# Kernel optimization log

Hardware: AMD Instinct MI355X
Metric: run time of the kernel (lower is better)

## Reference

```python
import jax, jax.numpy as jnp
import numpy as np

B, I, J, C = 1, 320, 320, 128
H, Dh = 4, 32
AH = H * Dh  # all_head_size == 128
EPS = 1e-5


def setup_inputs() -> dict:
    key = jax.random.key(0)
    ks = jax.random.split(key, 10)
    s = 0.05
    return {
        "z": jax.random.normal(ks[0], (B, I, J, C), jnp.float32),
        "z_mask": jax.random.randint(ks[1], (B, I, J), 0, 2, jnp.int32),
        "ln_scale": jnp.ones((C,), jnp.float32),
        "ln_bias": jnp.zeros((C,), jnp.float32),
        "Wq": jax.random.normal(ks[2], (C, AH), jnp.float32) * s,
        "Wk": jax.random.normal(ks[3], (C, AH), jnp.float32) * s,
        "Wv": jax.random.normal(ks[4], (C, AH), jnp.float32) * s,
        "Wg": jax.random.normal(ks[5], (C, AH), jnp.float32) * s,
        "bg": jnp.zeros((AH,), jnp.float32),
        "Wo": jax.random.normal(ks[6], (AH, C), jnp.float32) * s,
        "bo": jnp.zeros((C,), jnp.float32),
    }


def _layernorm(x, scale, bias):
    mu = jnp.mean(x, axis=-1, keepdims=True)
    var = jnp.var(x, axis=-1, keepdims=True)
    return (x - mu) * jax.lax.rsqrt(var + EPS) * scale + bias


def reference(z, z_mask, ln_scale, ln_bias, Wq, Wk, Wv, Wg, bg, Wo, bo):
    zn = _layernorm(z, ln_scale, ln_bias)                  # [B,I,J,C]
    m = z_mask.astype(jnp.float32)                         # [B,I,J]
    mask_bias = 1e9 * (m - 1.0)[:, :, None, None, :]       # [B,I,1,1,J]

    def heads(x):
        return x.reshape(x.shape[:-1] + (H, Dh))

    q = heads(zn @ Wq)                                     # [B,I,J,H,Dh]
    k = heads(zn @ Wk)
    v = heads(zn @ Wv)
    # NOTE: original module applies NO 1/sqrt(d) scaling — faithful.
    logits = jnp.einsum('biqhc,bikhc->bihqk', q, k) + mask_bias
    weights = jax.nn.softmax(logits, axis=-1)              # [B,I,H,J,J]
    wa = jnp.einsum('bihqk,bikhc->biqhc', weights, v)      # [B,I,J,H,Dh]
    g = jax.nn.sigmoid(heads(zn @ Wg + bg))                # [B,I,J,H,Dh]
    out = (g * wa).reshape(z.shape[:-1] + (AH,))           # [B,I,J,AH]
    return (out @ Wo + bo) * m[..., None]                  # [B,I,J,C]
```

## Files before the change

kernel.cpp:

```cpp
#include <hip/hip_runtime.h>

typedef _Float16 f16;
typedef _Float16 f16x2 __attribute__((ext_vector_type(2)));
typedef _Float16 f16x4 __attribute__((ext_vector_type(4)));
typedef _Float16 f16x8 __attribute__((ext_vector_type(8)));
typedef float f32x4 __attribute__((ext_vector_type(4)));

#define I_DIM 320
#define J_DIM 320
#define C_DIM 128
#define NROWS (I_DIM * J_DIM)
#define LOG2E 1.44269504f

__device__ inline float pkrtz(float a, float b) {
    return __builtin_bit_cast(float, __builtin_amdgcn_cvt_pkrtz(a, b));
}

__global__ __launch_bounds__(256) void prep_kernel(const float* __restrict__ Wq,
                                                   const float* __restrict__ Wk,
                                                   const float* __restrict__ Wv,
                                                   const float* __restrict__ Wg,
                                                   const float* __restrict__ Wo,
                                                   f16* __restrict__ Wfrag) {
    int f = blockIdx.x * 256 + threadIdx.x;
    int j = f & 7, lane = (f >> 3) & 63, n = (f >> 9) & 7;
    int ks = (f >> 12) & 3, w = f >> 14;
    int gq = lane >> 4, r16 = lane & 15;
    const float* W = (w == 0) ? Wq : (w == 1) ? Wk : (w == 2) ? Wv : (w == 3) ? Wg : Wo;
    float val = W[(size_t)(ks * 32 + gq * 8 + j) * 128 + n * 16 + r16];
    if (w == 0) val *= LOG2E;
    Wfrag[f] = (f16)val;
}

__global__ __launch_bounds__(256) void ln_kernel(const float* __restrict__ z,
                                                 const float* __restrict__ scale,
                                                 const float* __restrict__ bias,
                                                 f16* __restrict__ zn) {
    int s = blockIdx.x;
    int b = (s & 7) * 3200 + (s >> 3);
    int wave = threadIdx.x >> 6;
    int lane = threadIdx.x & 63;
    int row = b * 4 + wave;
    const float* zr = z + (size_t)row * C_DIM;
    float2 x = *(const float2*)(zr + lane * 2);
    float sm = x.x + x.y;
    float sq = x.x * x.x + x.y * x.y;
    #pragma unroll
    for (int o = 32; o; o >>= 1) {
        sm += __shfl_xor(sm, o);
        sq += __shfl_xor(sq, o);
    }
    float mu = sm * (1.0f / 128.0f);
    float var = sq * (1.0f / 128.0f) - mu * mu;
    float rs = rsqrtf(var + 1e-5f);
    int c0 = lane * 2;
    float y0 = (x.x - mu) * rs * scale[c0] + bias[c0];
    float y1 = (x.y - mu) * rs * scale[c0 + 1] + bias[c0 + 1];
    f16x2 o2 = {(f16)y0, (f16)y1};
    *(f16x2*)(zn + (size_t)row * C_DIM + c0) = o2;
}

__global__ __launch_bounds__(256, 3) void attn_mega(const f16* __restrict__ zn,
                                                    const f16* __restrict__ Wfrag,
                                                    const float* __restrict__ bg,
                                                    const int* __restrict__ z_mask,
                                                    f16* __restrict__ gwa) {
    __shared__ f16 Ksh[320][40];
    __shared__ f16 Vt[32][328];
    __shared__ float mbs[320];

    int bid = blockIdx.x;
    int xcd = bid & 7, idx = bid >> 3;
    int i = xcd * 40 + (idx >> 2);
    int h = idx & 3;
    size_t zbase = (size_t)i * (J_DIM * C_DIM);
    size_t gbase = zbase + h * 32;

    int wave = threadIdx.x >> 6;
    int lane = threadIdx.x & 63;
    int gq = lane >> 4, r16 = lane & 15;

    const f16* wfq = Wfrag;
    const f16* wfk = Wfrag + 16384;
    const f16* wfv = Wfrag + 32768;
    const f16* wfg = Wfrag + 49152;

    for (int t = threadIdx.x; t < 320; t += 256)
        mbs[t] = z_mask[i * J_DIM + t] ? -12.0f : -60000.0f;

    for (int rt = wave; rt < 20; rt += 4) {
        f16x8 a[4];
        #pragma unroll
        for (int ks = 0; ks < 4; ++ks)
            a[ks] = *(const f16x8*)(zn + zbase + (size_t)(rt * 16 + r16) * C_DIM + ks * 32 + gq * 8);
        f32x4 kacc[2] = {}, vacc[2] = {};
        #pragma unroll
        for (int ks = 0; ks < 4; ++ks) {
            #pragma unroll
            for (int n = 0; n < 2; ++n) {
                f16x8 bk = *(const f16x8*)(wfk + (ks * 8 + 2 * h + n) * 512 + lane * 8);
                kacc[n] = __builtin_amdgcn_mfma_f32_16x16x32_f16(a[ks], bk, kacc[n], 0, 0, 0);
                f16x8 bv = *(const f16x8*)(wfv + (ks * 8 + 2 * h + n) * 512 + lane * 8);
                vacc[n] = __builtin_amdgcn_mfma_f32_16x16x32_f16(a[ks], bv, vacc[n], 0, 0, 0);
            }
        }
        int kcol = (r16 >> 2) * 8 + (r16 & 3);
        int colbase = (rt >> 1) * 32 + gq * 8 + (rt & 1) * 4;
        #pragma unroll
        for (int n = 0; n < 2; ++n) {
            #pragma unroll
            for (int rr = 0; rr < 4; ++rr)
                Ksh[rt * 16 + gq * 4 + rr][kcol + 4 * n] = (f16)kacc[n][rr];
            f16x4 vp = {(f16)vacc[n][0], (f16)vacc[n][1], (f16)vacc[n][2], (f16)vacc[n][3]};
            *(f16x4*)(&Vt[n * 16 + r16][colbase]) = vp;
        }
    }
    __syncthreads();

    f16x8 qa[5];
    f32x4 gacc[5][2] = {};
    #pragma unroll
    for (int u = 0; u < 5; ++u) {
        int qt = u * 4 + wave;
        f16x8 a[4];
        #pragma unroll
        for (int ks = 0; ks < 4; ++ks)
            a[ks] = *(const f16x8*)(zn + zbase + (size_t)(qt * 16 + r16) * C_DIM + ks * 32 + gq * 8);
        f32x4 qacc[2] = {};
        #pragma unroll
        for (int ks = 0; ks < 4; ++ks) {
            #pragma unroll
            for (int n = 0; n < 2; ++n) {
                f16x8 bq = *(const f16x8*)(wfq + (ks * 8 + 2 * h + n) * 512 + lane * 8);
                qacc[n] = __builtin_amdgcn_mfma_f32_16x16x32_f16(bq, a[ks], qacc[n], 0, 0, 0);
                f16x8 bgf = *(const f16x8*)(wfg + (ks * 8 + 2 * h + n) * 512 + lane * 8);
                gacc[u][n] = __builtin_amdgcn_mfma_f32_16x16x32_f16(a[ks], bgf, gacc[u][n], 0, 0, 0);
            }
        }
        union { float f[4]; f16x8 v; } qu;
        qu.f[0] = pkrtz(qacc[0][0], qacc[0][1]);
        qu.f[1] = pkrtz(qacc[0][2], qacc[0][3]);
        qu.f[2] = pkrtz(qacc[1][0], qacc[1][1]);
        qu.f[3] = pkrtz(qacc[1][2], qacc[1][3]);
        qa[u] = qu.v;
    }

    const f16x8 ones = {(f16)1, (f16)1, (f16)1, (f16)1, (f16)1, (f16)1, (f16)1, (f16)1};
    f32x4 wa[5][2] = {};
    f32x4 wa2[5] = {};

    #pragma unroll 2
    for (int kc = 0; kc < 10; ++kc) {
        f16x8 kb0 = *(const f16x8*)(&Ksh[kc * 32 + r16][gq * 8]);
        f16x8 kb1 = *(const f16x8*)(&Ksh[kc * 32 + 16 + r16][gq * 8]);
        f32x4 mk0 = *(const f32x4*)(&mbs[kc * 32 + 4 * gq]);
        f32x4 mk1 = *(const f32x4*)(&mbs[kc * 32 + 16 + 4 * gq]);
        f16x8 vb0 = *(const f16x8*)(&Vt[r16][kc * 32 + gq * 8]);
        f16x8 vb1 = *(const f16x8*)(&Vt[16 + r16][kc * 32 + gq * 8]);
        #pragma unroll
        for (int u = 0; u < 5; ++u) {
            f32x4 sc0 = __builtin_amdgcn_mfma_f32_16x16x32_f16(kb0, qa[u], mk0, 0, 0, 0);
            f32x4 sc1 = __builtin_amdgcn_mfma_f32_16x16x32_f16(kb1, qa[u], mk1, 0, 0, 0);
            float p0[4], p1[4];
            #pragma unroll
            for (int r = 0; r < 4; ++r) {
                p0[r] = __builtin_amdgcn_exp2f(sc0[r]);
                p1[r] = __builtin_amdgcn_exp2f(sc1[r]);
            }
            union { float f[4]; f16x8 v; } pu;
            pu.f[0] = pkrtz(p0[0], p0[1]);
            pu.f[1] = pkrtz(p0[2], p0[3]);
            pu.f[2] = pkrtz(p1[0], p1[1]);
            pu.f[3] = pkrtz(p1[2], p1[3]);
            wa[u][0] = __builtin_amdgcn_mfma_f32_16x16x32_f16(pu.v, vb0, wa[u][0], 0, 0, 0);
            wa[u][1] = __builtin_amdgcn_mfma_f32_16x16x32_f16(pu.v, vb1, wa[u][1], 0, 0, 0);
            wa2[u]   = __builtin_amdgcn_mfma_f32_16x16x32_f16(pu.v, ones, wa2[u], 0, 0, 0);
        }
    }

    float bgv0 = bg[h * 32 + r16];
    float bgv1 = bg[h * 32 + 16 + r16];
    #pragma unroll
    for (int u = 0; u < 5; ++u) {
        int qt = u * 4 + wave;
        float rinv[4];
        #pragma unroll
        for (int r = 0; r < 4; ++r)
            rinv[r] = 1.0f / wa2[u][r];
        #pragma unroll
        for (int n = 0; n < 2; ++n) {
            float bgn = n ? bgv1 : bgv0;
            #pragma unroll
            for (int r = 0; r < 4; ++r) {
                int jq = qt * 16 + gq * 4 + r;
                int dh = n * 16 + r16;
                float gv = 1.0f / (1.0f + __expf(-(gacc[u][n][r] + bgn)));
                gwa[gbase + (size_t)jq * C_DIM + dh] = (f16)(gv * wa[u][n][r] * rinv[r]);
            }
        }
    }
}

__global__ __launch_bounds__(256) void out_kernel(const f16* __restrict__ gwa,
                                                  const f16* __restrict__ Wofrag,
                                                  const float* __restrict__ bo,
                                                  const int* __restrict__ z_mask,
                                                  float* __restrict__ out) {
    int s = blockIdx.x;
    int b = (s & 7) * 50 + (s >> 3);
    int wave = threadIdx.x >> 6;
    int lane = threadIdx.x & 63;
    int gq = lane >> 4, r16 = lane & 15;
    int row0 = b * 256 + wave * 64;

    f32x4 acc[4][8] = {};
    #pragma unroll
    for (int ks = 0; ks < 4; ++ks) {
        f16x8 a[4];
        #pragma unroll
        for (int m = 0; m < 4; ++m)
            a[m] = *(const f16x8*)(gwa + (size_t)(row0 + m * 16 + r16) * C_DIM + ks * 32 + gq * 8);
        #pragma unroll
        for (int n = 0; n < 8; ++n) {
            f16x8 bb = *(const f16x8*)(Wofrag + (ks * 8 + n) * 512 + lane * 8);
            #pragma unroll
            for (int m = 0; m < 4; ++m)
                acc[m][n] = __builtin_amdgcn_mfma_f32_16x16x32_f16(a[m], bb, acc[m][n], 0, 0, 0);
        }
    }
    #pragma unroll
    for (int m = 0; m < 4; ++m) {
        #pragma unroll
        for (int rr = 0; rr < 4; ++rr) {
            int row = row0 + m * 16 + gq * 4 + rr;
            float mk = (float)z_mask[row];
            #pragma unroll
            for (int n = 0; n < 8; ++n) {
                int col = n * 16 + r16;
                out[(size_t)row * C_DIM + col] = (acc[m][n][rr] + bo[col]) * mk;
            }
        }
    }
}

extern "C" void kernel_launch(void* const* d_in, const int* in_sizes, int n_in,
                              void* d_out, int out_size, void* d_ws, size_t ws_size,
                              hipStream_t stream) {
    const float* z        = (const float*)d_in[0];
    const int*   z_mask   = (const int*)d_in[1];
    const float* ln_scale = (const float*)d_in[2];
    const float* ln_bias  = (const float*)d_in[3];
    const float* Wq       = (const float*)d_in[4];
    const float* Wk       = (const float*)d_in[5];
    const float* Wv       = (const float*)d_in[6];
    const float* Wg       = (const float*)d_in[7];
    const float* bg       = (const float*)d_in[8];
    const float* Wo       = (const float*)d_in[9];
    const float* bo       = (const float*)d_in[10];
    float* out = (float*)d_out;

    char* ws = (char*)d_ws;
    const size_t SZ = (size_t)NROWS * C_DIM * sizeof(f16);
    f16* zn    = (f16*)(ws);
    f16* gwa   = (f16*)(ws + 1 * SZ);
    f16* Wfrag = (f16*)(ws + 2 * SZ);

    prep_kernel<<<320, 256, 0, stream>>>(Wq, Wk, Wv, Wg, Wo, Wfrag);
    ln_kernel  <<<NROWS / 4, 256, 0, stream>>>(z, ln_scale, ln_bias, zn);
    attn_mega  <<<I_DIM * 4, 256, 0, stream>>>(zn, Wfrag, bg, z_mask, gwa);
    out_kernel <<<NROWS / 256, 256, 0, stream>>>(gwa, Wfrag + 4 * 16384, bo, z_mask, out);
}
```

Measured before the change: 98.36 us.

## Fuse LayerNorm into attention kernel, computing MFMA fragments from fp32 z

Removes the standalone LayerNorm kernel and the fp16 zn workspace. The attention kernel now loads fp32 z rows directly and normalizes them in registers while building the MFMA A fragments, with scale and bias staged in shared memory. This drops one launch and a full write and reread of the normalized tensor. In exchange, each block reads twice as many bytes per row, redundantly recomputes LN statistics across the four head blocks and both passes, and raises register pressure.

```diff
diff --git a/kernel.cpp b/kernel.cpp
--- a/kernel.cpp
+++ b/kernel.cpp
@@ -14,6 +14,42 @@
 
 __device__ inline float pkrtz(float a, float b) {
     return __builtin_bit_cast(float, __builtin_amdgcn_cvt_pkrtz(a, b));
+}
+
+__device__ __forceinline__ void ln_frags(const float* __restrict__ zr,
+                                         const float* __restrict__ scf,
+                                         const float* __restrict__ bif,
+                                         int gq, f16x8 a[4]) {
+    float4 zv[8];
+    #pragma unroll
+    for (int ks = 0; ks < 4; ++ks) {
+        zv[2 * ks]     = *(const float4*)(zr + ks * 32 + gq * 8);
+        zv[2 * ks + 1] = *(const float4*)(zr + ks * 32 + gq * 8 + 4);
+    }
+    float s = 0.0f, sq = 0.0f;
+    #pragma unroll
+    for (int t = 0; t < 8; ++t) {
+        float4 v = zv[t];
+        s  += v.x + v.y + v.z + v.w;
+        sq += v.x * v.x + v.y * v.y + v.z * v.z + v.w * v.w;
+    }
+    s  += __shfl_xor(s, 16);  s  += __shfl_xor(s, 32);
+    sq += __shfl_xor(sq, 16); sq += __shfl_xor(sq, 32);
+    float mu = s * (1.0f / 128.0f);
+    float var = sq * (1.0f / 128.0f) - mu * mu;
+    float rs = rsqrtf(var + 1e-5f);
+    #pragma unroll
+    for (int ks = 0; ks < 4; ++ks) {
+        int c0 = ks * 32 + gq * 8;
+        f16x8 av;
+        #pragma unroll
+        for (int j = 0; j < 8; ++j) {
+            float zj = (j < 4) ? ((const float*)&zv[2 * ks])[j]
+                               : ((const float*)&zv[2 * ks + 1])[j - 4];
+            av[j] = (f16)((zj - mu) * rs * scf[c0 + j] + bif[c0 + j]);
+        }
+        a[ks] = av;
+    }
 }
 
 __global__ __launch_bounds__(256) void prep_kernel(const float* __restrict__ Wq,
@@ -32,35 +68,9 @@
     Wfrag[f] = (f16)val;
 }
 
-__global__ __launch_bounds__(256) void ln_kernel(const float* __restrict__ z,
-                                                 const float* __restrict__ scale,
-                                                 const float* __restrict__ bias,
-                                                 f16* __restrict__ zn) {
-    int s = blockIdx.x;
-    int b = (s & 7) * 3200 + (s >> 3);
-    int wave = threadIdx.x >> 6;
-    int lane = threadIdx.x & 63;
-    int row = b * 4 + wave;
-    const float* zr = z + (size_t)row * C_DIM;
-    float2 x = *(const float2*)(zr + lane * 2);
-    float sm = x.x + x.y;
-    float sq = x.x * x.x + x.y * x.y;
-    #pragma unroll
-    for (int o = 32; o; o >>= 1) {
-        sm += __shfl_xor(sm, o);
-        sq += __shfl_xor(sq, o);
-    }
-    float mu = sm * (1.0f / 128.0f);
-    float var = sq * (1.0f / 128.0f) - mu * mu;
-    float rs = rsqrtf(var + 1e-5f);
-    int c0 = lane * 2;
-    float y0 = (x.x - mu) * rs * scale[c0] + bias[c0];
-    float y1 = (x.y - mu) * rs * scale[c0 + 1] + bias[c0 + 1];
-    f16x2 o2 = {(f16)y0, (f16)y1};
-    *(f16x2*)(zn + (size_t)row * C_DIM + c0) = o2;
-}
-
-__global__ __launch_bounds__(256, 3) void attn_mega(const f16* __restrict__ zn,
+__global__ __launch_bounds__(256, 3) void attn_mega(const float* __restrict__ z,
+                                                    const float* __restrict__ ln_scale,
+                                                    const float* __restrict__ ln_bias,
                                                     const f16* __restrict__ Wfrag,
                                                     const float* __restrict__ bg,
                                                     const int* __restrict__ z_mask,
@@ -68,13 +78,14 @@
     __shared__ f16 Ksh[320][40];
     __shared__ f16 Vt[32][328];
     __shared__ float mbs[320];
+    __shared__ float scf[128];
+    __shared__ float bif[128];
 
     int bid = blockIdx.x;
     int xcd = bid & 7, idx = bid >> 3;
     int i = xcd * 40 + (idx >> 2);
     int h = idx & 3;
-    size_t zbase = (size_t)i * (J_DIM * C_DIM);
-    size_t gbase = zbase + h * 32;
+    size_t gbase = (size_t)i * (J_DIM * C_DIM) + h * 32;
 
     int wave = threadIdx.x >> 6;
     int lane = threadIdx.x & 63;
@@ -87,12 +98,16 @@
 
     for (int t = threadIdx.x; t < 320; t += 256)
         mbs[t] = z_mask[i * J_DIM + t] ? -12.0f : -60000.0f;
+    for (int t = threadIdx.x; t < 128; t += 256) {
+        scf[t] = ln_scale[t];
+        bif[t] = ln_bias[t];
+    }
+    __syncthreads();
 
     for (int rt = wave; rt < 20; rt += 4) {
+        const float* zr = z + ((size_t)i * J_DIM + rt * 16 + r16) * C_DIM;
         f16x8 a[4];
-        #pragma unroll
-        for (int ks = 0; ks < 4; ++ks)
-            a[ks] = *(const f16x8*)(zn + zbase + (size_t)(rt * 16 + r16) * C_DIM + ks * 32 + gq * 8);
+        ln_frags(zr, scf, bif, gq, a);
         f32x4 kacc[2] = {}, vacc[2] = {};
         #pragma unroll
         for (int ks = 0; ks < 4; ++ks) {
@@ -122,10 +137,9 @@
     #pragma unroll
     for (int u = 0; u < 5; ++u) {
         int qt = u * 4 + wave;
+        const float* zr = z + ((size_t)i * J_DIM + qt * 16 + r16) * C_DIM;
         f16x8 a[4];
-        #pragma unroll
-        for (int ks = 0; ks < 4; ++ks)
-            a[ks] = *(const f16x8*)(zn + zbase + (size_t)(qt * 16 + r16) * C_DIM + ks * 32 + gq * 8);
+        ln_frags(zr, scf, bif, gq, a);
         f32x4 qacc[2] = {};
         #pragma unroll
         for (int ks = 0; ks < 4; ++ks) {
@@ -261,12 +275,10 @@
 
     char* ws = (char*)d_ws;
     const size_t SZ = (size_t)NROWS * C_DIM * sizeof(f16);
-    f16* zn    = (f16*)(ws);
-    f16* gwa   = (f16*)(ws + 1 * SZ);
-    f16* Wfrag = (f16*)(ws + 2 * SZ);
+    f16* gwa   = (f16*)(ws);
+    f16* Wfrag = (f16*)(ws + SZ);
 
     prep_kernel<<<320, 256, 0, stream>>>(Wq, Wk, Wv, Wg, Wo, Wfrag);
-    ln_kernel  <<<NROWS / 4, 256, 0, stream>>>(z, ln_scale, ln_bias, zn);
-    attn_mega  <<<I_DIM * 4, 256, 0, stream>>>(zn, Wfrag, bg, z_mask, gwa);
+    attn_mega  <<<I_DIM * 4, 256, 0, stream>>>(z, ln_scale, ln_bias, Wfrag, bg, z_mask, gwa);
     out_kernel <<<NROWS / 256, 256, 0, stream>>>(gwa, Wfrag + 4 * 16384, bo, z_mask, out);
 }
```

After: 197.2 us. +100.5%, slower.
